# Kernel tuning notes

Measured on AMD Instinct MI355X. Metric: run time of the kernel, lower is better.

## Reference

```python
import jax, jax.numpy as jnp
import numpy as np
import math

DIM, HEADS = 512, 8
D_K = DIM // HEADS

def setup_inputs() -> dict:
    key = jax.random.key(0)
    ks = jax.random.split(key, 6)
    B, LK, LQ = 16, 2048, 256
    s = 1.0 / math.sqrt(DIM)
    return {
        "L": jax.random.normal(ks[0], (B, LK, DIM), jnp.float32),
        "G": jax.random.normal(ks[1], (B, LQ, DIM), jnp.float32),
        "Wq": jax.random.normal(ks[2], (DIM, DIM), jnp.float32) * s,
        "bq": jnp.zeros((DIM,), jnp.float32),
        "Wo": jax.random.normal(ks[3], (DIM, DIM), jnp.float32) * s,
        "bo": jnp.zeros((DIM,), jnp.float32),
    }

def reference(L, G, Wq, bq, Wo, bo):
    B = G.shape[0]
    # Q projection from global tokens; K,V are raw local features split into heads
    q = (G @ Wq + bq).reshape(B, -1, HEADS, D_K)          # [B, Lq, H, d]
    k = L.reshape(B, -1, HEADS, D_K)                      # [B, Lk, H, d]
    v = k
    # double scaling as in source: / sqrt(d_k) * dim**-0.5
    scale = (D_K ** -0.5) * (DIM ** -0.5)
    dots = jnp.einsum("bqhd,bkhd->bhqk", q, k) * scale    # [B, H, Lq, Lk]
    attn = jax.nn.softmax(dots, axis=-1)
    x = jnp.einsum("bhqk,bkhd->bqhd", attn, v)            # [B, Lq, H, d]
    x = x.reshape(B, -1, HEADS * D_K)
    return x @ Wo + bo
```

## Files before the change

### kernel.cpp

```cpp
#include <hip/hip_runtime.h>

#define KSTR 72

typedef __attribute__((ext_vector_type(8))) short short8;
typedef __attribute__((ext_vector_type(4))) float f32x4;

#define EXP2F(x) __builtin_amdgcn_exp2f(x)

__device__ __forceinline__ unsigned short f2bf(float f) {
    union { float f; unsigned u; } v; v.f = f;
    unsigned r = v.u + 0x7fff + ((v.u >> 16) & 1);
    return (unsigned short)(r >> 16);
}
__device__ __forceinline__ unsigned pk2(float a, float b) {
    return (unsigned)f2bf(a) | ((unsigned)f2bf(b) << 16);
}

__global__ __launch_bounds__(256) void conv_W(const float* __restrict__ Wq,
                                              const float* __restrict__ Wo,
                                              unsigned short* __restrict__ WqF,
                                              unsigned short* __restrict__ WoF) {
    const float* W = blockIdx.y ? Wo : Wq;
    unsigned short* WF = blockIdx.y ? WoF : WqF;
    int g = blockIdx.x * 256 + threadIdx.x;
    int lane = g & 63, ntg = (g >> 6) & 31, kt = g >> 11;
    int c = lane & 15, quad = lane >> 4;
    const float* wp = W + (size_t)(32 * kt + 8 * quad) * 512 + 16 * ntg + c;
    float v[8];
    #pragma unroll
    for (int j = 0; j < 8; j++) v[j] = wp[(size_t)j * 512];
    uint4 u;
    u.x = pk2(v[0], v[1]); u.y = pk2(v[2], v[3]);
    u.z = pk2(v[4], v[5]); u.w = pk2(v[6], v[7]);
    *(uint4*)(WF + (size_t)g * 8) = u;
}

__global__ __launch_bounds__(256) void conv_L(const float* __restrict__ Lmat,
                                              unsigned short* __restrict__ KF,
                                              unsigned short* __restrict__ VF) {
    __shared__ unsigned short KFs[4096];
    __shared__ unsigned short VFs[4096];
    const int blk = blockIdx.x;
    const int t = blk & 31, h = (blk >> 5) & 7, b = blk >> 8;
    const int tid = threadIdx.x;
    const int key = tid & 63, wv = tid >> 6;

    const float* src = Lmat + ((size_t)(b * 2048 + 64 * t + key)) * 512 + 64 * h + 16 * wv;
    float4 a0 = *(const float4*)src;
    float4 a1 = *(const float4*)(src + 4);
    float4 a2 = *(const float4*)(src + 8);
    float4 a3 = *(const float4*)(src + 12);
    float vals[16] = {a0.x, a0.y, a0.z, a0.w, a1.x, a1.y, a1.z, a1.w,
                      a2.x, a2.y, a2.z, a2.w, a3.x, a3.y, a3.z, a3.w};
    #pragma unroll
    for (int i = 0; i < 16; i++) {
        int d = 16 * wv + i;
        unsigned short bv = f2bf(vals[i]);
        KFs[((((key >> 4) * 2 + (d >> 5)) * 64) + ((d >> 3) & 3) * 16 + (key & 15)) * 8 + (d & 7)] = bv;
        VFs[((((d >> 4) * 2 + (key >> 5)) * 64) + ((key >> 3) & 3) * 16 + (d & 15)) * 8 + (key & 7)] = bv;
    }
    __syncthreads();
    size_t gbase = (size_t)blk * 4096 + tid * 16;
    *(uint4*)(KF + gbase)     = *(const uint4*)&KFs[tid * 16];
    *(uint4*)(KF + gbase + 8) = *(const uint4*)&KFs[tid * 16 + 8];
    *(uint4*)(VF + gbase)     = *(const uint4*)&VFs[tid * 16];
    *(uint4*)(VF + gbase + 8) = *(const uint4*)&VFs[tid * 16 + 8];
}

template<bool A_BF16, bool OUT_BF16>
__global__ __launch_bounds__(256) void gemm_direct(const void* __restrict__ Ap,
                                                   const unsigned short* __restrict__ WF,
                                                   const float* __restrict__ bias,
                                                   void* __restrict__ Cp,
                                                   float oscale) {
    const int tid = threadIdx.x;
    const int wv = tid >> 6, lane = tid & 63;
    const int c = lane & 15, quad = lane >> 4;
    const int m0 = blockIdx.x * 64, n0 = blockIdx.y * 64;
    const int row = m0 + 16 * wv + c;

    f32x4 acc[4];
    #pragma unroll
    for (int nt = 0; nt < 4; nt++) acc[nt] = (f32x4){0.f, 0.f, 0.f, 0.f};

    #pragma unroll
    for (int kk = 0; kk < 16; kk++) {
        short8 af;
        if (A_BF16) {
            af = *(const short8*)((const unsigned short*)Ap + (size_t)row * 512 + 32 * kk + 8 * quad);
        } else {
            const float* ap = (const float*)Ap + (size_t)row * 512 + 32 * kk + 8 * quad;
            float4 x0 = *(const float4*)ap;
            float4 x1 = *(const float4*)(ap + 4);
            af[0] = (short)f2bf(x0.x); af[1] = (short)f2bf(x0.y);
            af[2] = (short)f2bf(x0.z); af[3] = (short)f2bf(x0.w);
            af[4] = (short)f2bf(x1.x); af[5] = (short)f2bf(x1.y);
            af[6] = (short)f2bf(x1.z); af[7] = (short)f2bf(x1.w);
        }
        #pragma unroll
        for (int nt = 0; nt < 4; nt++) {
            short8 bf = *(const short8*)(WF +
                (((size_t)kk * 32 + (n0 >> 4) + nt) * 64 + lane) * 8);
            acc[nt] = __builtin_amdgcn_mfma_f32_16x16x32_bf16(af, bf, acc[nt], 0, 0, 0);
        }
    }

    #pragma unroll
    for (int nt = 0; nt < 4; nt++) {
        float bv = bias[n0 + 16 * nt + c];
        #pragma unroll
        for (int r = 0; r < 4; r++) {
            float v = (acc[nt][r] + bv) * oscale;
            size_t idx = (size_t)(m0 + 16 * wv + 4 * quad + r) * 512 + n0 + 16 * nt + c;
            if (OUT_BF16) ((unsigned short*)Cp)[idx] = f2bf(v);
            else          ((float*)Cp)[idx] = v;
        }
    }
}

__global__ __launch_bounds__(256) void attn_frag(const unsigned short* __restrict__ Q,
                                                 const unsigned short* __restrict__ KF,
                                                 const unsigned short* __restrict__ VF,
                                                 unsigned short* __restrict__ X) {
    __shared__ unsigned short Pw[4][16 * KSTR];

    const int raw = blockIdx.x;
    const int h  = raw & 7;
    const int qt = (raw >> 3) & 3;
    const int b  = raw >> 5;
    const int tid = threadIdx.x;
    const int wv = tid >> 6, lane = tid & 63;
    const int c = lane & 15, quad = lane >> 4;

    short8 qa[2];
    {
        const unsigned short* qsrc =
            Q + ((size_t)(b * 256 + qt * 64 + 16 * wv + c)) * 512 + h * 64;
        qa[0] = *(const short8*)(qsrc + 8 * quad);
        qa[1] = *(const short8*)(qsrc + 32 + 8 * quad);
    }
    short8 ones;
    #pragma unroll
    for (int i = 0; i < 8; i++) ones[i] = (short)0x3F80;

    f32x4 oacc[4];
    #pragma unroll
    for (int dt = 0; dt < 4; dt++) oacc[dt] = (f32x4){0.f, 0.f, 0.f, 0.f};
    f32x4 lacc = (f32x4){0.f, 0.f, 0.f, 0.f};

    const int swc = (c >> 3) & 1;
    const int swr = (quad >> 1) & 1;

    const unsigned short* kf = KF + ((size_t)((b * 8 + h) * 32)) * 4096 + lane * 8;
    const unsigned short* vf = VF + ((size_t)((b * 8 + h) * 32)) * 4096 + lane * 8;

    short8 kc[8], vc[8], kn[8], vn[8];
    #pragma unroll
    for (int f = 0; f < 8; f++) {
        kc[f] = *(const short8*)(kf + f * 512);
        vc[f] = *(const short8*)(vf + f * 512);
    }

    auto compute = [&](short8* kb, short8* vb) {
        f32x4 sacc[4];
        #pragma unroll
        for (int nt = 0; nt < 4; nt++) sacc[nt] = (f32x4){0.f, 0.f, 0.f, 0.f};
        #pragma unroll
        for (int nt = 0; nt < 4; nt++)
            #pragma unroll
            for (int ks = 0; ks < 2; ks++)
                sacc[nt] = __builtin_amdgcn_mfma_f32_16x16x32_bf16(
                    qa[ks], kb[nt * 2 + ks], sacc[nt], 0, 0, 0);
        #pragma unroll
        for (int nt = 0; nt < 4; nt++)
            #pragma unroll
            for (int r = 0; r < 4; r++)
                Pw[wv][(4 * quad + r) * KSTR + ((16 * nt + c) ^ (8 * swr))] =
                    f2bf(EXP2F(sacc[nt][r]));
        short8 pa0 = *(const short8*)&Pw[wv][c * KSTR + (8 * (quad ^ swc))];
        short8 pa1 = *(const short8*)&Pw[wv][c * KSTR + 32 + (8 * (quad ^ swc))];
        #pragma unroll
        for (int dt = 0; dt < 4; dt++) {
            oacc[dt] = __builtin_amdgcn_mfma_f32_16x16x32_bf16(pa0, vb[dt * 2], oacc[dt], 0, 0, 0);
            oacc[dt] = __builtin_amdgcn_mfma_f32_16x16x32_bf16(pa1, vb[dt * 2 + 1], oacc[dt], 0, 0, 0);
        }
        lacc = __builtin_amdgcn_mfma_f32_16x16x32_bf16(pa0, ones, lacc, 0, 0, 0);
        lacc = __builtin_amdgcn_mfma_f32_16x16x32_bf16(pa1, ones, lacc, 0, 0, 0);
    };

    for (int t = 0; t < 32; t += 2) {
        {
            const unsigned short* k2 = kf + (size_t)(t + 1) * 4096;
            const unsigned short* v2 = vf + (size_t)(t + 1) * 4096;
            #pragma unroll
            for (int f = 0; f < 8; f++) {
                kn[f] = *(const short8*)(k2 + f * 512);
                vn[f] = *(const short8*)(v2 + f * 512);
            }
        }
        compute(kc, vc);
        if (t + 2 < 32) {
            const unsigned short* k2 = kf + (size_t)(t + 2) * 4096;
            const unsigned short* v2 = vf + (size_t)(t + 2) * 4096;
            #pragma unroll
            for (int f = 0; f < 8; f++) {
                kc[f] = *(const short8*)(k2 + f * 512);
                vc[f] = *(const short8*)(v2 + f * 512);
            }
        }
        compute(kn, vn);
    }

    #pragma unroll
    for (int r = 0; r < 4; r++) {
        float inv = 1.f / lacc[r];
        size_t row = (size_t)(b * 256 + qt * 64 + 16 * wv + 4 * quad + r);
        unsigned short* xp = X + row * 512 + h * 64;
        #pragma unroll
        for (int dt = 0; dt < 4; dt++)
            xp[16 * dt + c] = f2bf(oacc[dt][r] * inv);
    }
}

extern "C" void kernel_launch(void* const* d_in, const int* in_sizes, int n_in,
                              void* d_out, int out_size, void* d_ws, size_t ws_size,
                              hipStream_t stream) {
    const float* Lmat = (const float*)d_in[0];
    const float* G    = (const float*)d_in[1];
    const float* Wq   = (const float*)d_in[2];
    const float* bq   = (const float*)d_in[3];
    const float* Wo   = (const float*)d_in[4];
    const float* bo   = (const float*)d_in[5];
    float* out = (float*)d_out;

    const float SCe = 0.005524271728019903f * 1.4426950408889634f;
    dim3 gg(64, 8);

    unsigned short* Qws = (unsigned short*)d_ws;
    unsigned short* Xws = Qws + (size_t)2097152;
    unsigned short* WqF = Xws + (size_t)2097152;
    unsigned short* WoF = WqF + (size_t)262144;
    unsigned short* KF  = WoF + (size_t)262144;
    unsigned short* VF  = KF  + (size_t)16777216;

    conv_W<<<dim3(128, 2), 256, 0, stream>>>(Wq, Wo, WqF, WoF);
    conv_L<<<4096, 256, 0, stream>>>(Lmat, KF, VF);
    gemm_direct<false, true><<<gg, 256, 0, stream>>>(G, WqF, bq, Qws, SCe);
    attn_frag<<<512, 256, 0, stream>>>(Qws, KF, VF, Xws);
    gemm_direct<true, false><<<gg, 256, 0, stream>>>(Xws, WoF, bo, out, 1.0f);
}
```

Before: 178.8 us.

## Stage K/V and weight tiles through double-buffered LDS shared across waves

```diff
diff --git a/kernel.cpp b/kernel.cpp
--- a/kernel.cpp
+++ b/kernel.cpp
@@ -68,42 +68,81 @@
 }
 
 template<bool A_BF16, bool OUT_BF16>
-__global__ __launch_bounds__(256) void gemm_direct(const void* __restrict__ Ap,
-                                                   const unsigned short* __restrict__ WF,
-                                                   const float* __restrict__ bias,
-                                                   void* __restrict__ Cp,
-                                                   float oscale) {
+__global__ __launch_bounds__(256) void gemm_v3(const void* __restrict__ Ap,
+                                               const unsigned short* __restrict__ WF,
+                                               const float* __restrict__ bias,
+                                               void* __restrict__ Cp,
+                                               float oscale) {
+    __shared__ __align__(16) unsigned short Bs[2][4096];
+
     const int tid = threadIdx.x;
     const int wv = tid >> 6, lane = tid & 63;
     const int c = lane & 15, quad = lane >> 4;
     const int m0 = blockIdx.x * 64, n0 = blockIdx.y * 64;
     const int row = m0 + 16 * wv + c;
+    const int half = tid >> 7;
+    const int toff = (tid & 127) * 16;
 
     f32x4 acc[4];
     #pragma unroll
     for (int nt = 0; nt < 4; nt++) acc[nt] = (f32x4){0.f, 0.f, 0.f, 0.f};
 
-    #pragma unroll
-    for (int kk = 0; kk < 16; kk++) {
-        short8 af;
-        if (A_BF16) {
-            af = *(const short8*)((const unsigned short*)Ap + (size_t)row * 512 + 32 * kk + 8 * quad);
-        } else {
-            const float* ap = (const float*)Ap + (size_t)row * 512 + 32 * kk + 8 * quad;
-            float4 x0 = *(const float4*)ap;
-            float4 x1 = *(const float4*)(ap + 4);
-            af[0] = (short)f2bf(x0.x); af[1] = (short)f2bf(x0.y);
-            af[2] = (short)f2bf(x0.z); af[3] = (short)f2bf(x0.w);
-            af[4] = (short)f2bf(x1.x); af[5] = (short)f2bf(x1.y);
-            af[6] = (short)f2bf(x1.z); af[7] = (short)f2bf(x1.w);
-        }
-        #pragma unroll
-        for (int nt = 0; nt < 4; nt++) {
-            short8 bf = *(const short8*)(WF +
-                (((size_t)kk * 32 + (n0 >> 4) + nt) * 64 + lane) * 8);
-            acc[nt] = __builtin_amdgcn_mfma_f32_16x16x32_bf16(af, bf, acc[nt], 0, 0, 0);
-        }
-    }
+    short8 afc[2], afn[2];
+    uint4 br0, br1;
+
+    #define LOAD_A(s, dst)                                                          \
+        {                                                                           \
+            _Pragma("unroll")                                                       \
+            for (int kkl = 0; kkl < 2; kkl++) {                                     \
+                if (A_BF16) {                                                       \
+                    dst[kkl] = *(const short8*)((const unsigned short*)Ap +         \
+                        (size_t)row * 512 + 64 * (s) + 32 * kkl + 8 * quad);        \
+                } else {                                                            \
+                    const float* ap_ = (const float*)Ap +                           \
+                        (size_t)row * 512 + 64 * (s) + 32 * kkl + 8 * quad;         \
+                    float4 x0 = *(const float4*)ap_;                                \
+                    float4 x1 = *(const float4*)(ap_ + 4);                          \
+                    dst[kkl][0] = (short)f2bf(x0.x); dst[kkl][1] = (short)f2bf(x0.y);\
+                    dst[kkl][2] = (short)f2bf(x0.z); dst[kkl][3] = (short)f2bf(x0.w);\
+                    dst[kkl][4] = (short)f2bf(x1.x); dst[kkl][5] = (short)f2bf(x1.y);\
+                    dst[kkl][6] = (short)f2bf(x1.z); dst[kkl][7] = (short)f2bf(x1.w);\
+                }                                                                   \
+            }                                                                       \
+        }
+    #define LOAD_B(s)                                                               \
+        {                                                                           \
+            const unsigned short* src_ = WF +                                       \
+                ((size_t)((2 * (s) + half) * 32 + (n0 >> 4))) * 512 + toff;         \
+            br0 = *(const uint4*)src_;                                              \
+            br1 = *(const uint4*)(src_ + 8);                                        \
+        }
+
+    LOAD_A(0, afc);
+    LOAD_B(0);
+    *(uint4*)&Bs[0][(half << 11) + toff]     = br0;
+    *(uint4*)&Bs[0][(half << 11) + toff + 8] = br1;
+    __syncthreads();
+
+    int p = 0;
+    for (int s = 0; s < 8; s++) {
+        if (s < 7) { LOAD_B(s + 1); LOAD_A(s + 1, afn); }
+        #pragma unroll
+        for (int kkl = 0; kkl < 2; kkl++)
+            #pragma unroll
+            for (int nt = 0; nt < 4; nt++) {
+                short8 bf = *(const short8*)&Bs[p][(kkl << 11) + (nt << 9) + lane * 8];
+                acc[nt] = __builtin_amdgcn_mfma_f32_16x16x32_bf16(afc[kkl], bf, acc[nt], 0, 0, 0);
+            }
+        if (s < 7) {
+            *(uint4*)&Bs[p ^ 1][(half << 11) + toff]     = br0;
+            *(uint4*)&Bs[p ^ 1][(half << 11) + toff + 8] = br1;
+            afc[0] = afn[0]; afc[1] = afn[1];
+        }
+        __syncthreads();
+        p ^= 1;
+    }
+    #undef LOAD_A
+    #undef LOAD_B
 
     #pragma unroll
     for (int nt = 0; nt < 4; nt++) {
@@ -122,7 +161,9 @@
                                                  const unsigned short* __restrict__ KF,
                                                  const unsigned short* __restrict__ VF,
                                                  unsigned short* __restrict__ X) {
-    __shared__ unsigned short Pw[4][16 * KSTR];
+    __shared__ __align__(16) unsigned short Ks[2][4096];
+    __shared__ __align__(16) unsigned short Vs[2][4096];
+    __shared__ __align__(16) unsigned short Pw[4][16 * KSTR];
 
     const int raw = blockIdx.x;
     const int h  = raw & 7;
@@ -151,26 +192,44 @@
     const int swc = (c >> 3) & 1;
     const int swr = (quad >> 1) & 1;
 
-    const unsigned short* kf = KF + ((size_t)((b * 8 + h) * 32)) * 4096 + lane * 8;
-    const unsigned short* vf = VF + ((size_t)((b * 8 + h) * 32)) * 4096 + lane * 8;
-
-    short8 kc[8], vc[8], kn[8], vn[8];
-    #pragma unroll
-    for (int f = 0; f < 8; f++) {
-        kc[f] = *(const short8*)(kf + f * 512);
-        vc[f] = *(const short8*)(vf + f * 512);
-    }
-
-    auto compute = [&](short8* kb, short8* vb) {
+    const unsigned short* kfT = KF + ((size_t)((b * 8 + h) * 32)) * 4096 + tid * 16;
+    const unsigned short* vfT = VF + ((size_t)((b * 8 + h) * 32)) * 4096 + tid * 16;
+
+    {
+        uint4 k0 = *(const uint4*)kfT;
+        uint4 k1 = *(const uint4*)(kfT + 8);
+        uint4 v0 = *(const uint4*)vfT;
+        uint4 v1 = *(const uint4*)(vfT + 8);
+        *(uint4*)&Ks[0][tid * 16]     = k0;
+        *(uint4*)&Ks[0][tid * 16 + 8] = k1;
+        *(uint4*)&Vs[0][tid * 16]     = v0;
+        *(uint4*)&Vs[0][tid * 16 + 8] = v1;
+    }
+    __syncthreads();
+
+    int p = 0;
+    for (int t = 0; t < 32; t++) {
+        uint4 ka, kb2, va, vb2;
+        if (t < 31) {
+            const unsigned short* ksrc = kfT + (size_t)(t + 1) * 4096;
+            const unsigned short* vsrc = vfT + (size_t)(t + 1) * 4096;
+            ka  = *(const uint4*)ksrc;
+            kb2 = *(const uint4*)(ksrc + 8);
+            va  = *(const uint4*)vsrc;
+            vb2 = *(const uint4*)(vsrc + 8);
+        }
+
         f32x4 sacc[4];
         #pragma unroll
         for (int nt = 0; nt < 4; nt++) sacc[nt] = (f32x4){0.f, 0.f, 0.f, 0.f};
         #pragma unroll
         for (int nt = 0; nt < 4; nt++)
             #pragma unroll
-            for (int ks = 0; ks < 2; ks++)
-                sacc[nt] = __builtin_amdgcn_mfma_f32_16x16x32_bf16(
-                    qa[ks], kb[nt * 2 + ks], sacc[nt], 0, 0, 0);
+            for (int ksl = 0; ksl < 2; ksl++) {
+                short8 kbf = *(const short8*)&Ks[p][((nt << 1) + ksl) * 512 + lane * 8];
+                sacc[nt] = __builtin_amdgcn_mfma_f32_16x16x32_bf16(qa[ksl], kbf, sacc[nt], 0, 0, 0);
+            }
+
         #pragma unroll
         for (int nt = 0; nt < 4; nt++)
             #pragma unroll
@@ -179,36 +238,25 @@
                     f2bf(EXP2F(sacc[nt][r]));
         short8 pa0 = *(const short8*)&Pw[wv][c * KSTR + (8 * (quad ^ swc))];
         short8 pa1 = *(const short8*)&Pw[wv][c * KSTR + 32 + (8 * (quad ^ swc))];
+
         #pragma unroll
         for (int dt = 0; dt < 4; dt++) {
-            oacc[dt] = __builtin_amdgcn_mfma_f32_16x16x32_bf16(pa0, vb[dt * 2], oacc[dt], 0, 0, 0);
-            oacc[dt] = __builtin_amdgcn_mfma_f32_16x16x32_bf16(pa1, vb[dt * 2 + 1], oacc[dt], 0, 0, 0);
+            short8 v0 = *(const short8*)&Vs[p][((dt << 1) + 0) * 512 + lane * 8];
+            oacc[dt] = __builtin_amdgcn_mfma_f32_16x16x32_bf16(pa0, v0, oacc[dt], 0, 0, 0);
+            short8 v1 = *(const short8*)&Vs[p][((dt << 1) + 1) * 512 + lane * 8];
+            oacc[dt] = __builtin_amdgcn_mfma_f32_16x16x32_bf16(pa1, v1, oacc[dt], 0, 0, 0);
         }
         lacc = __builtin_amdgcn_mfma_f32_16x16x32_bf16(pa0, ones, lacc, 0, 0, 0);
         lacc = __builtin_amdgcn_mfma_f32_16x16x32_bf16(pa1, ones, lacc, 0, 0, 0);
-    };
-
-    for (int t = 0; t < 32; t += 2) {
-        {
-            const unsigned short* k2 = kf + (size_t)(t + 1) * 4096;
-            const unsigned short* v2 = vf + (size_t)(t + 1) * 4096;
-            #pragma unroll
-            for (int f = 0; f < 8; f++) {
-                kn[f] = *(const short8*)(k2 + f * 512);
-                vn[f] = *(const short8*)(v2 + f * 512);
-            }
-        }
-        compute(kc, vc);
-        if (t + 2 < 32) {
-            const unsigned short* k2 = kf + (size_t)(t + 2) * 4096;
-            const unsigned short* v2 = vf + (size_t)(t + 2) * 4096;
-            #pragma unroll
-            for (int f = 0; f < 8; f++) {
-                kc[f] = *(const short8*)(k2 + f * 512);
-                vc[f] = *(const short8*)(v2 + f * 512);
-            }
-        }
-        compute(kn, vn);
+
+        if (t < 31) {
+            *(uint4*)&Ks[p ^ 1][tid * 16]     = ka;
+            *(uint4*)&Ks[p ^ 1][tid * 16 + 8] = kb2;
+            *(uint4*)&Vs[p ^ 1][tid * 16]     = va;
+            *(uint4*)&Vs[p ^ 1][tid * 16 + 8] = vb2;
+        }
+        __syncthreads();
+        p ^= 1;
     }
 
     #pragma unroll
@@ -245,7 +293,7 @@
 
     conv_W<<<dim3(128, 2), 256, 0, stream>>>(Wq, Wo, WqF, WoF);
     conv_L<<<4096, 256, 0, stream>>>(Lmat, KF, VF);
-    gemm_direct<false, true><<<gg, 256, 0, stream>>>(G, WqF, bq, Qws, SCe);
+    gemm_v3<false, true><<<gg, 256, 0, stream>>>(G, WqF, bq, Qws, SCe);
     attn_frag<<<512, 256, 0, stream>>>(Qws, KF, VF, Xws);
-    gemm_direct<true, false><<<gg, 256, 0, stream>>>(Xws, WoF, bo, out, 1.0f);
-}
+    gemm_v3<true, false><<<gg, 256, 0, stream>>>(Xws, WoF, bo, out, 1.0f);
+}
```

Result: no change. 179.9 us (+0.6%).
